# Performance work log

Measured on AMD Instinct MI355X. Metric: run time of the kernel, lower is better.

The kernel has to match this reference:

```python
import jax, jax.numpy as jnp
import numpy as np

LMAX = 2
MMAX = 2
SPH = (LMAX + 1) ** 2  # 9 coefficients
E = 800000


def _rot_y(a):
    c, s = jnp.cos(a), jnp.sin(a)
    o, z = jnp.ones_like(a), jnp.zeros_like(a)
    return jnp.stack([jnp.stack([c, z, s], -1),
                      jnp.stack([z, o, z], -1),
                      jnp.stack([-s, z, c], -1)], -2)


def _rot_x(a):
    c, s = jnp.cos(a), jnp.sin(a)
    o, z = jnp.ones_like(a), jnp.zeros_like(a)
    return jnp.stack([jnp.stack([o, z, z], -1),
                      jnp.stack([z, c, -s], -1),
                      jnp.stack([z, s, c], -1)], -2)


def _z_rot_mat(angle, l):
    # e3nn _z_rot_mat: M[i, dim-1-i] = sin(f_i*angle); M[i, i] = cos(f_i*angle)
    dim = 2 * l + 1
    freqs = jnp.arange(l, -l - 1, -1, dtype=angle.dtype)  # (dim,)
    s = jnp.sin(freqs * angle[:, None])  # [E, dim]
    c = jnp.cos(freqs * angle[:, None])
    inds = jnp.arange(dim)
    M = jnp.zeros((angle.shape[0], dim, dim), angle.dtype)
    M = M.at[:, inds, dim - 1 - inds].set(s)
    M = M.at[:, inds, inds].set(c)  # center overwrites sin(0)=0, as in torch
    return M


def _wigner_D(l, alpha, beta, gamma, J):
    Xa = _z_rot_mat(alpha, l)
    Xb = _z_rot_mat(beta, l)
    Xc = _z_rot_mat(gamma, l)
    return Xa @ J @ Xb @ J @ Xc


def _build_to_m():
    # CoefficientMapping.to_m: permutation regrouping (l,m) coefficients by m
    idx = lambda l, m: l * l + l + m
    order = []
    for m in range(MMAX + 1):
        for l in range(m, LMAX + 1):
            order.append(idx(l, m))
        if m > 0:
            for l in range(m, LMAX + 1):
                order.append(idx(l, -m))
    to_m = np.zeros((SPH, SPH), np.float32)
    for row, col in enumerate(order):
        to_m[row, col] = 1.0
    return jnp.asarray(to_m)


def setup_inputs() -> dict:
    key = jax.random.key(0)
    k1, k2, k3, k4 = jax.random.split(key, 4)
    return {
        'edge_distance_vec': jax.random.normal(k1, (E, 3), jnp.float32),
        'rand_vec': jax.random.uniform(k2, (E, 3), jnp.float32),
        'Jd_1': jax.random.normal(k3, (3, 3), jnp.float32),
        'Jd_2': jax.random.normal(k4, (5, 5), jnp.float32),
        'to_m': _build_to_m(),
    }


def reference(edge_distance_vec, rand_vec, Jd_1, Jd_2, to_m):
    v = edge_distance_vec
    dtype = v.dtype
    # ---- init_edge_rot_mat (rot_clip=False since direct_forces=True) ----
    norm_x = v / jnp.linalg.norm(v, axis=1, keepdims=True)
    e2 = rand_vec - 0.5
    e2 = e2 / jnp.linalg.norm(e2, axis=1, keepdims=True)
    e2b = jnp.stack([-e2[:, 1], e2[:, 0], e2[:, 2]], axis=1)
    e2c = jnp.stack([e2[:, 0], -e2[:, 2], e2[:, 1]], axis=1)
    dot = lambda a: jnp.abs(jnp.sum(a * norm_x, axis=1, keepdims=True))
    e2 = jnp.where(dot(e2) > dot(e2b), e2b, e2)
    e2 = jnp.where(dot(e2) > dot(e2c), e2c, e2)
    norm_z = jnp.cross(norm_x, e2)
    norm_z = norm_z / jnp.linalg.norm(norm_z, axis=1, keepdims=True)
    norm_y = jnp.cross(norm_x, norm_z)
    norm_y = norm_y / jnp.linalg.norm(norm_y, axis=1, keepdims=True)
    R = jnp.stack([norm_z, norm_x, norm_y], axis=1)  # [E,3,3] rows z,x,y

    # ---- rotation_to_wigner: Euler angles (e3nn convention) ----
    x = R[:, :, 1]  # R @ e_y
    alpha = jnp.arctan2(x[:, 0], x[:, 2])
    beta = jnp.arccos(jnp.clip(x[:, 1], -1.0, 1.0))
    Ralign = _rot_y(alpha) @ _rot_x(beta) @ _rot_y(jnp.zeros_like(alpha))
    Rg = jnp.swapaxes(Ralign, 1, 2) @ R
    gamma = jnp.arctan2(Rg[:, 0, 2], Rg[:, 0, 0])

    Jd_0 = jnp.ones((1, 1), dtype)
    wigner = jnp.zeros((v.shape[0], SPH, SPH), dtype)
    start = 0
    for l, J in enumerate([Jd_0, Jd_1, Jd_2]):
        block = _wigner_D(l, alpha, beta, gamma, J.astype(dtype))
        wigner = wigner.at[:, start:start + 2 * l + 1,
                           start:start + 2 * l + 1].set(block)
        start += 2 * l + 1
    wigner_inv = jnp.swapaxes(wigner, 1, 2)  # lmax == mmax: no index_select

    wm = jnp.einsum('mk,nkj->nmj', to_m, wigner)
    wm_inv = jnp.einsum('njk,mk->njm', wigner_inv, to_m)
    return R, wm, wm_inv
```

## Files before the change

### kernel.cpp

```cpp
#include <hip/hip_runtime.h>
#include <hip/hip_bf16.h>
#include <math.h>

#define TPB 64

template<int DIM>
__device__ __forceinline__ void zchain(
    const float* __restrict__ J,
    const float (&ca)[DIM], const float (&sa)[DIM],
    const float (&cb)[DIM], const float (&sb)[DIM],
    const float (&cc)[DIM], const float (&sc)[DIM],
    float (&D)[DIM][DIM])
{
    constexpr int d1 = DIM - 1;
    float Jl[DIM][DIM];
#pragma unroll
    for (int i = 0; i < DIM; ++i)
#pragma unroll
        for (int j = 0; j < DIM; ++j)
            Jl[i][j] = J[i * DIM + j];

    float U[DIM][DIM];
#pragma unroll
    for (int i = 0; i < DIM; ++i)
#pragma unroll
        for (int j = 0; j < DIM; ++j)
            U[i][j] = ca[i] * Jl[i][j] + sa[i] * Jl[d1 - i][j];

    float V[DIM][DIM];
#pragma unroll
    for (int i = 0; i < DIM; ++i)
#pragma unroll
        for (int j = 0; j < DIM; ++j)
            V[i][j] = U[i][j] * cb[j] + U[i][d1 - j] * sb[d1 - j];

    float W[DIM][DIM];
#pragma unroll
    for (int i = 0; i < DIM; ++i)
#pragma unroll
        for (int j = 0; j < DIM; ++j) {
            float acc = 0.f;
#pragma unroll
            for (int k = 0; k < DIM; ++k)
                acc = fmaf(V[i][k], Jl[k][j], acc);
            W[i][j] = acc;
        }
#pragma unroll
    for (int i = 0; i < DIM; ++i)
#pragma unroll
        for (int j = 0; j < DIM; ++j)
            D[i][j] = W[i][j] * cc[j] + W[i][d1 - j] * sc[d1 - j];
}

__global__ __launch_bounds__(TPB) void wigner_kernel(
    const float* __restrict__ vec, const float* __restrict__ rnd,
    const float* __restrict__ J1,  const float* __restrict__ J2,
    const float* __restrict__ tom,
    float* __restrict__ outR,
    float* __restrict__ outWm,
    float* __restrict__ outWi,
    int E)
{
    __shared__ __align__(16) float lds[TPB * 81];
    __shared__ int invp[9];

    const int t  = threadIdx.x;
    const int e0 = blockIdx.x * TPB;
    const int e  = e0 + t;
    const int ei = (e < E) ? e : (E - 1);
    const int nvalid = min(TPB, E - e0);

    if (t < 9) {
        int p = 0;
#pragma unroll
        for (int k = 0; k < 9; ++k)
            if (tom[t * 9 + k] > 0.5f) p = k;
        invp[p] = t;
    }

    float vx = vec[3 * ei + 0], vy = vec[3 * ei + 1], vz = vec[3 * ei + 2];
    float rn = rsqrtf(vx * vx + vy * vy + vz * vz);
    float nx0 = vx * rn, nx1 = vy * rn, nx2 = vz * rn;

    float ox = rnd[3 * ei + 0] - 0.5f;
    float oy = rnd[3 * ei + 1] - 0.5f;
    float oz = rnd[3 * ei + 2] - 0.5f;
    float ro = rsqrtf(ox * ox + oy * oy + oz * oz);
    ox *= ro; oy *= ro; oz *= ro;

    float sx = ox, sy = oy, sz = oz;
    float dcur = fabsf(sx * nx0 + sy * nx1 + sz * nx2);
    {
        float bx = -oy, by = ox, bz = oz;
        float db = fabsf(bx * nx0 + by * nx1 + bz * nx2);
        if (dcur > db) { sx = bx; sy = by; sz = bz; dcur = db; }
        float cx = ox, cy = -oz, cz = oy;
        float dc = fabsf(cx * nx0 + cy * nx1 + cz * nx2);
        if (dcur > dc) { sx = cx; sy = cy; sz = cz; }
    }

    float zx = nx1 * sz - nx2 * sy;
    float zy = nx2 * sx - nx0 * sz;
    float zz = nx0 * sy - nx1 * sx;
    float rz = rsqrtf(zx * zx + zy * zy + zz * zz);
    zx *= rz; zy *= rz; zz *= rz;

    float yx = nx1 * zz - nx2 * zy;
    float yy = nx2 * zx - nx0 * zz;
    float yz = nx0 * zy - nx1 * zx;
    float ry = rsqrtf(yx * yx + yy * yy + yz * yz);
    yx *= ry; yy *= ry; yz *= ry;

    float alpha = atan2f(zy, yy);
    float beta  = acosf(fminf(1.f, fmaxf(-1.f, nx1)));
    float sa, caa, sb, cbb, sg, cgg;
    sincosf(alpha, &sa, &caa);
    sincosf(beta,  &sb, &cbb);
    float gamma = atan2f(caa * zz - sa * yz, caa * zx - sa * yx);
    sincosf(gamma, &sg, &cgg);

    float ca3[3] = {caa, 1.f, caa}, sa3[3] = {sa, 0.f, -sa};
    float cb3[3] = {cbb, 1.f, cbb}, sb3[3] = {sb, 0.f, -sb};
    float cc3[3] = {cgg, 1.f, cgg}, sc3[3] = {sg, 0.f, -sg};
    float D1[3][3];
    zchain<3>(J1, ca3, sa3, cb3, sb3, cc3, sc3, D1);

    float ca2 = caa * caa - sa * sa,  sa2 = 2.f * sa * caa;
    float cb2 = cbb * cbb - sb * sb,  sb2 = 2.f * sb * cbb;
    float cg2 = cgg * cgg - sg * sg,  sg2 = 2.f * sg * cgg;
    float ca5[5] = {ca2, caa, 1.f, caa, ca2}, sa5[5] = {sa2, sa, 0.f, -sa, -sa2};
    float cb5[5] = {cb2, cbb, 1.f, cbb, cb2}, sb5[5] = {sb2, sb, 0.f, -sb, -sb2};
    float cc5[5] = {cg2, cgg, 1.f, cgg, cg2}, sc5[5] = {sg2, sg, 0.f, -sg, -sg2};
    float D2[5][5];
    zchain<5>(J2, ca5, sa5, cb5, sb5, cc5, sc5, D2);

    {
        float* r9 = &lds[t * 9];
        r9[0] = zx;  r9[1] = zy;  r9[2] = zz;
        r9[3] = nx0; r9[4] = nx1; r9[5] = nx2;
        r9[6] = yx;  r9[7] = yy;  r9[8] = yz;
    }
    __syncthreads();
    if (nvalid == TPB) {
        const float4* s4 = reinterpret_cast<const float4*>(lds);
        float4* d4 = reinterpret_cast<float4*>(outR + (size_t)e0 * 9);
        for (int idx = t; idx < (TPB * 9) / 4; idx += TPB) d4[idx] = s4[idx];
    } else {
        float* d = outR + (size_t)e0 * 9;
        for (int idx = t; idx < nvalid * 9; idx += TPB) d[idx] = lds[idx];
    }
    __syncthreads();

    {
        float* w = &lds[t * 81];
#pragma unroll
        for (int k = 0; k < 81; ++k) w[k] = 0.f;
        w[invp[0] * 9 + 0] = 1.f;
#pragma unroll
        for (int r = 0; r < 3; ++r) {
            int m = invp[1 + r];
#pragma unroll
            for (int c = 0; c < 3; ++c)
                w[m * 9 + (1 + c)] = D1[r][c];
        }
#pragma unroll
        for (int r = 0; r < 5; ++r) {
            int m = invp[4 + r];
#pragma unroll
            for (int c = 0; c < 5; ++c)
                w[m * 9 + (4 + c)] = D2[r][c];
        }
    }
    __syncthreads();
    if (nvalid == TPB) {
        const float4* s4 = reinterpret_cast<const float4*>(lds);
        float4* d4 = reinterpret_cast<float4*>(outWm + (size_t)e0 * 81);
        for (int idx = t; idx < (TPB * 81) / 4; idx += TPB) d4[idx] = s4[idx];
    } else {
        float* d = outWm + (size_t)e0 * 81;
        for (int idx = t; idx < nvalid * 81; idx += TPB) d[idx] = lds[idx];
    }
    __syncthreads();

    {
        float* w = &lds[t * 81];
#pragma unroll
        for (int k = 0; k < 81; ++k) w[k] = 0.f;
        w[0 * 9 + invp[0]] = 1.f;
#pragma unroll
        for (int r = 0; r < 3; ++r) {
            int m = invp[1 + r];
#pragma unroll
            for (int c = 0; c < 3; ++c)
                w[(1 + c) * 9 + m] = D1[r][c];
        }
#pragma unroll
        for (int r = 0; r < 5; ++r) {
            int m = invp[4 + r];
#pragma unroll
            for (int c = 0; c < 5; ++c)
                w[(4 + c) * 9 + m] = D2[r][c];
        }
    }
    __syncthreads();
    if (nvalid == TPB) {
        const float4* s4 = reinterpret_cast<const float4*>(lds);
        float4* d4 = reinterpret_cast<float4*>(outWi + (size_t)e0 * 81);
        for (int idx = t; idx < (TPB * 81) / 4; idx += TPB) d4[idx] = s4[idx];
    } else {
        float* d = outWi + (size_t)e0 * 81;
        for (int idx = t; idx < nvalid * 81; idx += TPB) d[idx] = lds[idx];
    }
}

extern "C" void kernel_launch(void* const* d_in, const int* in_sizes, int n_in,
                              void* d_out, int out_size, void* d_ws, size_t ws_size,
                              hipStream_t stream) {
    const float* vec = (const float*)d_in[0];
    const float* rnd = (const float*)d_in[1];
    const float* J1  = (const float*)d_in[2];
    const float* J2  = (const float*)d_in[3];
    const float* tom = (const float*)d_in[4];
    float* out = (float*)d_out;

    const int E = in_sizes[0] / 3;
    float* outR  = out;
    float* outWm = out + (size_t)E * 9;
    float* outWi = out + (size_t)E * 90;

    const int blocks = (E + TPB - 1) / TPB;
    hipLaunchKernelGGL(wigner_kernel, dim3(blocks), dim3(TPB), 0, stream,
                       vec, rnd, J1, J2, tom, outR, outWm, outWi, E);
}
```

Baseline: 118.2 us.

## Hardcode to_m permutation, replace trig with rsqrt, merge staging, nontemporal stores

The kernel no longer reads the to_m input. It hardcodes the fixed permutation into compile-time LDS writes, which removes the dynamic-indexed scatter and the full zeroing passes. The atan2/acos/sincos chain is replaced by computing cosines and sines directly from normalized vector components with rsqrt. R and Wm get separate LDS buffers, so one sync phase is dropped, and all global writes now use nontemporal vector stores. Hardcoding to_m assumes the permutation input never changes, and the algebraic angle path handles near-degenerate edges differently.

```diff
diff --git a/kernel.cpp b/kernel.cpp
--- a/kernel.cpp
+++ b/kernel.cpp
@@ -3,6 +3,8 @@
 #include <math.h>
 
 #define TPB 64
+
+typedef float f32x4 __attribute__((ext_vector_type(4)));
 
 template<int DIM>
 __device__ __forceinline__ void zchain(
@@ -52,31 +54,23 @@
             D[i][j] = W[i][j] * cc[j] + W[i][d1 - j] * sc[d1 - j];
 }
 
+
 __global__ __launch_bounds__(TPB) void wigner_kernel(
     const float* __restrict__ vec, const float* __restrict__ rnd,
     const float* __restrict__ J1,  const float* __restrict__ J2,
-    const float* __restrict__ tom,
     float* __restrict__ outR,
     float* __restrict__ outWm,
     float* __restrict__ outWi,
     int E)
 {
-    __shared__ __align__(16) float lds[TPB * 81];
-    __shared__ int invp[9];
+    __shared__ __align__(16) float ldsR[TPB * 9];
+    __shared__ __align__(16) float ldsW[TPB * 81];
 
     const int t  = threadIdx.x;
     const int e0 = blockIdx.x * TPB;
     const int e  = e0 + t;
     const int ei = (e < E) ? e : (E - 1);
     const int nvalid = min(TPB, E - e0);
-
-    if (t < 9) {
-        int p = 0;
-#pragma unroll
-        for (int k = 0; k < 9; ++k)
-            if (tom[t * 9 + k] > 0.5f) p = k;
-        invp[p] = t;
-    }
 
     float vx = vec[3 * ei + 0], vy = vec[3 * ei + 1], vz = vec[3 * ei + 2];
     float rn = rsqrtf(vx * vx + vy * vy + vz * vz);
@@ -111,13 +105,20 @@
     float ry = rsqrtf(yx * yx + yy * yy + yz * yz);
     yx *= ry; yy *= ry; yz *= ry;
 
-    float alpha = atan2f(zy, yy);
-    float beta  = acosf(fminf(1.f, fmaxf(-1.f, nx1)));
-    float sa, caa, sb, cbb, sg, cgg;
-    sincosf(alpha, &sa, &caa);
-    sincosf(beta,  &sb, &cbb);
-    float gamma = atan2f(caa * zz - sa * yz, caa * zx - sa * yx);
-    sincosf(gamma, &sg, &cgg);
+    float h2a = zy * zy + yy * yy;
+    float rha = rsqrtf(fmaxf(h2a, 1e-30f));
+    bool  za  = (h2a < 1e-24f);
+    float sa  = za ? 0.f : zy * rha;
+    float caa = za ? 1.f : yy * rha;
+    float cbb = fminf(1.f, fmaxf(-1.f, nx1));
+    float sb  = sqrtf(fmaxf(0.f, 1.f - cbb * cbb));
+    float gy  = caa * zz - sa * yz;
+    float gx  = caa * zx - sa * yx;
+    float h2g = gy * gy + gx * gx;
+    float rhg = rsqrtf(fmaxf(h2g, 1e-30f));
+    bool  zg  = (h2g < 1e-24f);
+    float sg  = zg ? 0.f : gy * rhg;
+    float cgg = zg ? 1.f : gx * rhg;
 
     float ca3[3] = {caa, 1.f, caa}, sa3[3] = {sa, 0.f, -sa};
     float cb3[3] = {cbb, 1.f, cbb}, sb3[3] = {sb, 0.f, -sb};
@@ -135,81 +136,94 @@
     zchain<5>(J2, ca5, sa5, cb5, sb5, cc5, sc5, D2);
 
     {
-        float* r9 = &lds[t * 9];
+        float* r9 = &ldsR[t * 9];
         r9[0] = zx;  r9[1] = zy;  r9[2] = zz;
         r9[3] = nx0; r9[4] = nx1; r9[5] = nx2;
         r9[6] = yx;  r9[7] = yy;  r9[8] = yz;
+
+        float* w = &ldsW[t * 81];
+        w[0] = 1.f;
+#pragma unroll
+        for (int c = 1; c < 9; ++c) w[c] = 0.f;
+        w[9]  = 0.f; w[10] = D1[1][0]; w[11] = D1[1][1]; w[12] = D1[1][2];
+#pragma unroll
+        for (int c = 4; c < 9; ++c) w[9 + c] = 0.f;
+#pragma unroll
+        for (int c = 0; c < 4; ++c) w[18 + c] = 0.f;
+#pragma unroll
+        for (int c = 0; c < 5; ++c) w[22 + c] = D2[2][c];
+        w[27] = 0.f; w[28] = D1[2][0]; w[29] = D1[2][1]; w[30] = D1[2][2];
+#pragma unroll
+        for (int c = 4; c < 9; ++c) w[27 + c] = 0.f;
+#pragma unroll
+        for (int c = 0; c < 4; ++c) w[36 + c] = 0.f;
+#pragma unroll
+        for (int c = 0; c < 5; ++c) w[40 + c] = D2[3][c];
+        w[45] = 0.f; w[46] = D1[0][0]; w[47] = D1[0][1]; w[48] = D1[0][2];
+#pragma unroll
+        for (int c = 4; c < 9; ++c) w[45 + c] = 0.f;
+#pragma unroll
+        for (int c = 0; c < 4; ++c) w[54 + c] = 0.f;
+#pragma unroll
+        for (int c = 0; c < 5; ++c) w[58 + c] = D2[1][c];
+#pragma unroll
+        for (int c = 0; c < 4; ++c) w[63 + c] = 0.f;
+#pragma unroll
+        for (int c = 0; c < 5; ++c) w[67 + c] = D2[4][c];
+#pragma unroll
+        for (int c = 0; c < 4; ++c) w[72 + c] = 0.f;
+#pragma unroll
+        for (int c = 0; c < 5; ++c) w[76 + c] = D2[0][c];
     }
     __syncthreads();
+
     if (nvalid == TPB) {
-        const float4* s4 = reinterpret_cast<const float4*>(lds);
-        float4* d4 = reinterpret_cast<float4*>(outR + (size_t)e0 * 9);
-        for (int idx = t; idx < (TPB * 9) / 4; idx += TPB) d4[idx] = s4[idx];
+        const f32x4* sR = reinterpret_cast<const f32x4*>(ldsR);
+        f32x4* dR = reinterpret_cast<f32x4*>(outR + (size_t)e0 * 9);
+#pragma unroll
+        for (int idx = t; idx < (TPB * 9) / 4; idx += TPB)
+            __builtin_nontemporal_store(sR[idx], &dR[idx]);
+        const f32x4* sW = reinterpret_cast<const f32x4*>(ldsW);
+        f32x4* dW = reinterpret_cast<f32x4*>(outWm + (size_t)e0 * 81);
+        for (int idx = t; idx < (TPB * 81) / 4; idx += TPB)
+            __builtin_nontemporal_store(sW[idx], &dW[idx]);
     } else {
-        float* d = outR + (size_t)e0 * 9;
-        for (int idx = t; idx < nvalid * 9; idx += TPB) d[idx] = lds[idx];
+        float* dR = outR + (size_t)e0 * 9;
+        for (int idx = t; idx < nvalid * 9; idx += TPB) dR[idx] = ldsR[idx];
+        float* dW = outWm + (size_t)e0 * 81;
+        for (int idx = t; idx < nvalid * 81; idx += TPB) dW[idx] = ldsW[idx];
     }
     __syncthreads();
 
     {
-        float* w = &lds[t * 81];
-#pragma unroll
-        for (int k = 0; k < 81; ++k) w[k] = 0.f;
-        w[invp[0] * 9 + 0] = 1.f;
-#pragma unroll
-        for (int r = 0; r < 3; ++r) {
-            int m = invp[1 + r];
-#pragma unroll
-            for (int c = 0; c < 3; ++c)
-                w[m * 9 + (1 + c)] = D1[r][c];
+        float* w = &ldsW[t * 81];
+        w[0] = 1.f;
+#pragma unroll
+        for (int c = 1; c < 9; ++c) w[c] = 0.f;
+#pragma unroll
+        for (int j = 0; j < 3; ++j) {
+            float* r = &w[(1 + j) * 9];
+            r[0] = 0.f; r[1] = D1[1][j]; r[2] = 0.f; r[3] = D1[2][j];
+            r[4] = 0.f; r[5] = D1[0][j]; r[6] = 0.f; r[7] = 0.f; r[8] = 0.f;
         }
 #pragma unroll
-        for (int r = 0; r < 5; ++r) {
-            int m = invp[4 + r];
-#pragma unroll
-            for (int c = 0; c < 5; ++c)
-                w[m * 9 + (4 + c)] = D2[r][c];
+        for (int c = 0; c < 5; ++c) {
+            float* r = &w[(4 + c) * 9];
+            r[0] = 0.f; r[1] = 0.f; r[2] = D2[2][c]; r[3] = 0.f;
+            r[4] = D2[3][c]; r[5] = 0.f; r[6] = D2[1][c];
+            r[7] = D2[4][c]; r[8] = D2[0][c];
         }
     }
     __syncthreads();
+
     if (nvalid == TPB) {
-        const float4* s4 = reinterpret_cast<const float4*>(lds);
-        float4* d4 = reinterpret_cast<float4*>(outWm + (size_t)e0 * 81);
-        for (int idx = t; idx < (TPB * 81) / 4; idx += TPB) d4[idx] = s4[idx];
+        const f32x4* sW = reinterpret_cast<const f32x4*>(ldsW);
+        f32x4* dW = reinterpret_cast<f32x4*>(outWi + (size_t)e0 * 81);
+        for (int idx = t; idx < (TPB * 81) / 4; idx += TPB)
+            __builtin_nontemporal_store(sW[idx], &dW[idx]);
     } else {
-        float* d = outWm + (size_t)e0 * 81;
-        for (int idx = t; idx < nvalid * 81; idx += TPB) d[idx] = lds[idx];
-    }
-    __syncthreads();
-
-    {
-        float* w = &lds[t * 81];
-#pragma unroll
-        for (int k = 0; k < 81; ++k) w[k] = 0.f;
-        w[0 * 9 + invp[0]] = 1.f;
-#pragma unroll
-        for (int r = 0; r < 3; ++r) {
-            int m = invp[1 + r];
-#pragma unroll
-            for (int c = 0; c < 3; ++c)
-                w[(1 + c) * 9 + m] = D1[r][c];
-        }
-#pragma unroll
-        for (int r = 0; r < 5; ++r) {
-            int m = invp[4 + r];
-#pragma unroll
-            for (int c = 0; c < 5; ++c)
-                w[(4 + c) * 9 + m] = D2[r][c];
-        }
-    }
-    __syncthreads();
-    if (nvalid == TPB) {
-        const float4* s4 = reinterpret_cast<const float4*>(lds);
-        float4* d4 = reinterpret_cast<float4*>(outWi + (size_t)e0 * 81);
-        for (int idx = t; idx < (TPB * 81) / 4; idx += TPB) d4[idx] = s4[idx];
-    } else {
-        float* d = outWi + (size_t)e0 * 81;
-        for (int idx = t; idx < nvalid * 81; idx += TPB) d[idx] = lds[idx];
+        float* dW = outWi + (size_t)e0 * 81;
+        for (int idx = t; idx < nvalid * 81; idx += TPB) dW[idx] = ldsW[idx];
     }
 }
 
@@ -220,7 +234,6 @@
     const float* rnd = (const float*)d_in[1];
     const float* J1  = (const float*)d_in[2];
     const float* J2  = (const float*)d_in[3];
-    const float* tom = (const float*)d_in[4];
     float* out = (float*)d_out;
 
     const int E = in_sizes[0] / 3;
@@ -230,5 +243,5 @@
 
     const int blocks = (E + TPB - 1) / TPB;
     hipLaunchKernelGGL(wigner_kernel, dim3(blocks), dim3(TPB), 0, stream,
-                       vec, rnd, J1, J2, tom, outR, outWm, outWi, E);
+                       vec, rnd, J1, J2, outR, outWm, outWi, E);
 }
```

Result: faster. 108.4 us (-8.4%).
